# Kernel tuning notes

Hardware: AMD Instinct MI355X
Metric: run time of the kernel (lower is better)

The kernel has to match this reference:

```python
import jax, jax.numpy as jnp
import numpy as np

# Llama-7B FFN up-proj quantized with HQQ 4-bit, group_size=64, axis=0
OUT, IN, GS = 11008, 4096, 64
G = OUT * IN // GS  # 704512 groups


def setup_inputs() -> dict:
    key = jax.random.key(0)
    k1, k2, k3, k4, k5 = jax.random.split(key, 5)
    # packed 4-bit weights: two nibbles per byte, shape [GS//2, G]
    W_q = jax.random.randint(k1, (GS // 2, G), 0, 256, dtype=jnp.int32)
    # per-group scale (meta['scale'] = 1/scale from quantize) and zero
    scale = jax.random.uniform(k2, (1, G), jnp.float32, minval=1e-3, maxval=1e-2)
    zero = jax.random.uniform(k3, (1, G), jnp.float32, minval=0.0, maxval=15.0)
    # decode-style activations: 8 sequences, 1 token each
    x = jax.random.normal(k4, (8, 1, IN), dtype=jnp.float32)
    bias = jax.random.normal(k5, (OUT,), dtype=jnp.float32) * 0.01
    return {"W_q": W_q, "scale": scale, "zero": zero, "x": x, "bias": bias}


def reference(W_q, scale, zero, x, bias):
    # BitPack.unpack_4bit_u8: high nibble rows stacked on low nibble rows
    hi = (W_q >> 4) & 0xF
    lo = W_q & 0xF
    W_q_p = jnp.concatenate([hi, lo], axis=0).astype(x.dtype)  # [GS, G]
    # Quantizer.dequantize: (W_q_p - zero) * scale, reshape to weight shape
    W_r = ((W_q_p - zero) * scale).reshape(OUT, IN)  # [out, in]
    # torch.nn.functional.linear(x, W_r, bias)
    return jnp.einsum('bsi,oi->bso', x, W_r) + bias
```

## Files before the change

### kernel.cpp

```cpp
#include <hip/hip_runtime.h>


#define OUT_ 11008
#define IN_ 4096
#define G_ 704512
#define OC_ 172
#define KS 4
#define KC (IN_ / KS)
#define ITERS (KC / 256)
#define SIB (OC_ * KS)
#define NB (4 * SIB)

__global__ __launch_bounds__(256, 4)
void hqq_gemv(const int* __restrict__ Wq, const float* __restrict__ scale,
              const float* __restrict__ zero, const float* __restrict__ x,
              float* __restrict__ ws) {
    __shared__ float red[128 * 64];

    const int lane = threadIdx.x;
    const int ty   = threadIdx.y;
    const int bid  = blockIdx.x;
    const int bx   = bid / SIB;
    const int rem  = bid % SIB;
    const int oc   = rem >> 2;
    const int ks   = rem & 3;
    const int rq0  = bx * 8 + ty * 2;

    const int kbase = ks * KC;
    const int gb = oc * IN_ + kbase;

    const int* __restrict__ wqA = Wq + (long)rq0 * G_ + gb;
    const int* __restrict__ wqB = wqA + G_;
    int4 qA[ITERS], qB[ITERS];
#pragma unroll
    for (int it = 0; it < ITERS; ++it) {
        qA[it] = *(const int4*)(wqA + it * 256 + lane * 4);
        qB[it] = *(const int4*)(wqB + it * 256 + lane * 4);
    }

    float acc[4][8];
#pragma unroll
    for (int r = 0; r < 4; ++r)
#pragma unroll
        for (int b = 0; b < 8; ++b) acc[r][b] = 0.f;

#pragma unroll
    for (int it = 0; it < ITERS; ++it) {
        const int i = it * 256 + lane * 4;
        const float4 s4 = *(const float4*)(scale + gb + i);
        const float4 z4 = *(const float4*)(zero + gb + i);
        const float ss[4] = {s4.x, s4.y, s4.z, s4.w};
        const float zs[4] = {-z4.x * s4.x, -z4.y * s4.y, -z4.z * s4.z, -z4.w * s4.w};
        const int qsA[4] = {qA[it].x, qA[it].y, qA[it].z, qA[it].w};
        const int qsB[4] = {qB[it].x, qB[it].y, qB[it].z, qB[it].w};

        float w[4][4];
#pragma unroll
        for (int j = 0; j < 4; ++j) {
            w[0][j] = fmaf((float)((qsA[j] >> 4) & 0xF), ss[j], zs[j]);
            w[1][j] = fmaf((float)( qsA[j]       & 0xF), ss[j], zs[j]);
            w[2][j] = fmaf((float)((qsB[j] >> 4) & 0xF), ss[j], zs[j]);
            w[3][j] = fmaf((float)( qsB[j]       & 0xF), ss[j], zs[j]);
        }
#pragma unroll
        for (int b = 0; b < 8; ++b) {
            const float4 xb = *(const float4*)(x + b * IN_ + kbase + i);
#pragma unroll
            for (int r = 0; r < 4; ++r) {
                float a = acc[r][b];
                a = fmaf(xb.x, w[r][0], a);
                a = fmaf(xb.y, w[r][1], a);
                a = fmaf(xb.z, w[r][2], a);
                a = fmaf(xb.w, w[r][3], a);
                acc[r][b] = a;
            }
        }
    }

    const int obase = ty * 32;
#pragma unroll
    for (int r = 0; r < 4; ++r)
#pragma unroll
        for (int b = 0; b < 8; ++b) {
            const int o = obase + r * 8 + b;
            red[o * 64 + (lane ^ ((o & 7) << 3))] = acc[r][b];
        }
    __syncthreads();

    const int t = ty * 64 + lane;
    if (t < 128) {
        const int o = t;
        const int c = (o & 7) << 3;
        float s = 0.f;
#pragma unroll
        for (int j = 0; j < 16; ++j) {
            const float4 v = *(const float4*)(red + o * 64 + ((j * 4) ^ c));
            s += (v.x + v.y) + (v.z + v.w);
        }
        const int w_  = o >> 5;
        const int r   = (o >> 3) & 3;
        const int b   = o & 7;
        const int rq  = bx * 8 + w_ * 2 + (r >> 1);
        const int row = rq + ((r & 1) ? 32 : 0);
        ws[((long)ks * 8 + b) * OUT_ + row * OC_ + oc] = s;
    }
}

__global__ void hqq_reduce(const float* __restrict__ ws,
                           const float* __restrict__ bias,
                           float* __restrict__ out) {
    const int t = blockIdx.x * 256 + threadIdx.x;
    if (t >= 8 * OUT_) return;
    const int o = t % OUT_;
    float v = bias[o];
#pragma unroll
    for (int k = 0; k < KS; ++k) v += ws[k * 8 * OUT_ + t];
    out[t] = v;
}

extern "C" void kernel_launch(void* const* d_in, const int* in_sizes, int n_in,
                              void* d_out, int out_size, void* d_ws, size_t ws_size,
                              hipStream_t stream) {
    const int*   Wq    = (const int*)d_in[0];
    const float* scale = (const float*)d_in[1];
    const float* zero  = (const float*)d_in[2];
    const float* x     = (const float*)d_in[3];
    const float* bias  = (const float*)d_in[4];
    float* out = (float*)d_out;
    float* ws  = (float*)d_ws;

    dim3 grid(NB);
    dim3 block(64, 4);
    hqq_gemv<<<grid, block, 0, stream>>>(Wq, scale, zero, x, ws);
    hqq_reduce<<<(8 * OUT_ + 255) / 256, 256, 0, stream>>>(ws, bias, out);
}
```

Baseline: 152.2 us.

## Stage x, scale, zero into LDS via async global_load_lds and coalesce partial writes

Loads the activation slice, scale and zero vectors into shared memory with the direct global-to-LDS load builtin before the main loop, so the per-wave loads that were repeated across the four waves become one shared copy. The LDS buffer is reused for the cross-lane reduction with a modified XOR swizzle. Partial-sum writes become contiguous per block, and the reduce kernel takes over the scattered index mapping. This adds a block-wide barrier and a larger LDS footprint (40KB), which may reduce occupancy below the launch-bounds target.

```diff
diff --git a/kernel.cpp b/kernel.cpp
--- a/kernel.cpp
+++ b/kernel.cpp
@@ -11,14 +11,24 @@
 #define SIB (OC_ * KS)
 #define NB (4 * SIB)
 
+typedef const __attribute__((address_space(1))) void* gptr1_t;
+typedef __attribute__((address_space(3))) void* sptr3_t;
+
+__device__ __forceinline__ void gload_lds16(const float* g, float* l) {
+    __builtin_amdgcn_global_load_lds((gptr1_t)g, (sptr3_t)l, 16, 0, 0);
+}
+
 __global__ __launch_bounds__(256, 4)
 void hqq_gemv(const int* __restrict__ Wq, const float* __restrict__ scale,
               const float* __restrict__ zero, const float* __restrict__ x,
               float* __restrict__ ws) {
-    __shared__ float red[128 * 64];
+    __shared__ float x_lds[8 * KC];
+    __shared__ float s_lds[KC];
+    __shared__ float z_lds[KC];
 
     const int lane = threadIdx.x;
     const int ty   = threadIdx.y;
+    const int tid  = ty * 64 + lane;
     const int bid  = blockIdx.x;
     const int bx   = bid / SIB;
     const int rem  = bid % SIB;
@@ -29,6 +39,14 @@
     const int kbase = ks * KC;
     const int gb = oc * IN_ + kbase;
 
+    const int wf = ty * 256;
+    gload_lds16(scale + gb + wf + lane * 4, s_lds + wf);
+    gload_lds16(zero  + gb + wf + lane * 4, z_lds + wf);
+#pragma unroll
+    for (int r = 0; r < 8; ++r) {
+        gload_lds16(x + r * IN_ + kbase + wf + lane * 4, x_lds + r * 1024 + wf);
+    }
+
     const int* __restrict__ wqA = Wq + (long)rq0 * G_ + gb;
     const int* __restrict__ wqB = wqA + G_;
     int4 qA[ITERS], qB[ITERS];
@@ -37,6 +55,8 @@
         qA[it] = *(const int4*)(wqA + it * 256 + lane * 4);
         qB[it] = *(const int4*)(wqB + it * 256 + lane * 4);
     }
+
+    __syncthreads();
 
     float acc[4][8];
 #pragma unroll
@@ -47,8 +67,8 @@
 #pragma unroll
     for (int it = 0; it < ITERS; ++it) {
         const int i = it * 256 + lane * 4;
-        const float4 s4 = *(const float4*)(scale + gb + i);
-        const float4 z4 = *(const float4*)(zero + gb + i);
+        const float4 s4 = *(const float4*)(s_lds + i);
+        const float4 z4 = *(const float4*)(z_lds + i);
         const float ss[4] = {s4.x, s4.y, s4.z, s4.w};
         const float zs[4] = {-z4.x * s4.x, -z4.y * s4.y, -z4.z * s4.z, -z4.w * s4.w};
         const int qsA[4] = {qA[it].x, qA[it].y, qA[it].z, qA[it].w};
@@ -64,7 +84,7 @@
         }
 #pragma unroll
         for (int b = 0; b < 8; ++b) {
-            const float4 xb = *(const float4*)(x + b * IN_ + kbase + i);
+            const float4 xb = *(const float4*)(x_lds + b * KC + i);
 #pragma unroll
             for (int r = 0; r < 4; ++r) {
                 float a = acc[r][b];
@@ -77,32 +97,28 @@
         }
     }
 
+    float* red = x_lds;
+    __syncthreads();
     const int obase = ty * 32;
 #pragma unroll
     for (int r = 0; r < 4; ++r)
 #pragma unroll
         for (int b = 0; b < 8; ++b) {
             const int o = obase + r * 8 + b;
-            red[o * 64 + (lane ^ ((o & 7) << 3))] = acc[r][b];
+            red[o * 64 + (lane ^ ((o & 7) << 2))] = acc[r][b];
         }
     __syncthreads();
 
-    const int t = ty * 64 + lane;
-    if (t < 128) {
-        const int o = t;
-        const int c = (o & 7) << 3;
+    if (tid < 128) {
+        const int o = tid;
+        const int c = (o & 7) << 2;
         float s = 0.f;
 #pragma unroll
         for (int j = 0; j < 16; ++j) {
             const float4 v = *(const float4*)(red + o * 64 + ((j * 4) ^ c));
             s += (v.x + v.y) + (v.z + v.w);
         }
-        const int w_  = o >> 5;
-        const int r   = (o >> 3) & 3;
-        const int b   = o & 7;
-        const int rq  = bx * 8 + w_ * 2 + (r >> 1);
-        const int row = rq + ((r & 1) ? 32 : 0);
-        ws[((long)ks * 8 + b) * OUT_ + row * OC_ + oc] = s;
+        ws[(long)((bx * OC_ + oc) * KS + ks) * 128 + o] = s;
     }
 }
 
@@ -112,9 +128,18 @@
     const int t = blockIdx.x * 256 + threadIdx.x;
     if (t >= 8 * OUT_) return;
     const int o = t % OUT_;
+    const int b = t / OUT_;
+    const int row = o / OC_;
+    const int oc  = o % OC_;
+    const int rq  = row & 31;
+    const int hi  = row >> 5;
+    const int bx  = rq >> 3;
+    const int w_  = (rq >> 1) & 3;
+    const int r   = ((rq & 1) << 1) | hi;
+    const int base = ((bx * OC_ + oc) * KS) * 128 + w_ * 32 + r * 8 + b;
     float v = bias[o];
 #pragma unroll
-    for (int k = 0; k < KS; ++k) v += ws[k * 8 * OUT_ + t];
+    for (int k = 0; k < KS; ++k) v += ws[base + k * 128];
     out[t] = v;
 }
 
```

After: 144.9 us (median of 3 runs). 1.05x faster.

## Use single-wave blocks with XCD-aware chunk mapping and double-buffered loads

Applied to the files above, without the earlier changes.

Shrinks each block to one 64-thread wave and remaps block ids so that all 16 row-pair waves sharing a (oc, ks) chunk land on the same XCD. The aim is for them to share scale, zero and x data in that XCD's L2. The up-front load of every weight vector is replaced by a two-stage register double buffer that also prefetches scale and zero. The workspace layout changes to be chunk-major, so the reduce kernel now recovers output indices itself. This trades more, smaller blocks and less memory-level parallelism per wave for better L2 locality and lower register pressure.

```diff
diff --git a/kernel.cpp b/kernel.cpp
--- a/kernel.cpp
+++ b/kernel.cpp
@@ -8,35 +8,40 @@
 #define KS 4
 #define KC (IN_ / KS)
 #define ITERS (KC / 256)
-#define SIB (OC_ * KS)
-#define NB (4 * SIB)
+#define NCHUNK (OC_ * KS)
+#define NB (NCHUNK * 16)
 
-__global__ __launch_bounds__(256, 4)
+__global__ __launch_bounds__(64, 4)
 void hqq_gemv(const int* __restrict__ Wq, const float* __restrict__ scale,
               const float* __restrict__ zero, const float* __restrict__ x,
               float* __restrict__ ws) {
-    __shared__ float red[128 * 64];
+    __shared__ float red[32 * 64];
 
     const int lane = threadIdx.x;
-    const int ty   = threadIdx.y;
     const int bid  = blockIdx.x;
-    const int bx   = bid / SIB;
-    const int rem  = bid % SIB;
-    const int oc   = rem >> 2;
-    const int ks   = rem & 3;
-    const int rq0  = bx * 8 + ty * 2;
+    const int xcd  = bid & 7;
+    const int i_   = bid >> 3;
+    const int c    = xcd * (NCHUNK / 8) + (i_ >> 4);
+    const int sib  = i_ & 15;
+    const int oc   = c >> 2;
+    const int ks   = c & 3;
+    const int rq0  = sib * 2;
 
     const int kbase = ks * KC;
-    const int gb = oc * IN_ + kbase;
+    const int gb    = oc * IN_ + kbase;
 
-    const int* __restrict__ wqA = Wq + (long)rq0 * G_ + gb;
-    const int* __restrict__ wqB = wqA + G_;
-    int4 qA[ITERS], qB[ITERS];
-#pragma unroll
-    for (int it = 0; it < ITERS; ++it) {
-        qA[it] = *(const int4*)(wqA + it * 256 + lane * 4);
-        qB[it] = *(const int4*)(wqB + it * 256 + lane * 4);
-    }
+    const int*   __restrict__ wqA = Wq + (long)rq0 * G_ + gb + lane * 4;
+    const int*   __restrict__ wqB = wqA + G_;
+    const float* __restrict__ sp  = scale + gb + lane * 4;
+    const float* __restrict__ zp  = zero  + gb + lane * 4;
+    const float* __restrict__ xp  = x + kbase + lane * 4;
+
+    int4   qa[2], qb[2];
+    float4 sv[2], zv[2];
+    qa[0] = *(const int4*)(wqA);
+    qb[0] = *(const int4*)(wqB);
+    sv[0] = *(const float4*)(sp);
+    zv[0] = *(const float4*)(zp);
 
     float acc[4][8];
 #pragma unroll
@@ -46,13 +51,19 @@
 
 #pragma unroll
     for (int it = 0; it < ITERS; ++it) {
-        const int i = it * 256 + lane * 4;
-        const float4 s4 = *(const float4*)(scale + gb + i);
-        const float4 z4 = *(const float4*)(zero + gb + i);
+        const int cur = it & 1, nxt = cur ^ 1;
+        if (it + 1 < ITERS) {
+            qa[nxt] = *(const int4*)(wqA + (it + 1) * 256);
+            qb[nxt] = *(const int4*)(wqB + (it + 1) * 256);
+            sv[nxt] = *(const float4*)(sp + (it + 1) * 256);
+            zv[nxt] = *(const float4*)(zp + (it + 1) * 256);
+        }
+        const float4 s4 = sv[cur];
+        const float4 z4 = zv[cur];
         const float ss[4] = {s4.x, s4.y, s4.z, s4.w};
         const float zs[4] = {-z4.x * s4.x, -z4.y * s4.y, -z4.z * s4.z, -z4.w * s4.w};
-        const int qsA[4] = {qA[it].x, qA[it].y, qA[it].z, qA[it].w};
-        const int qsB[4] = {qB[it].x, qB[it].y, qB[it].z, qB[it].w};
+        const int qsA[4] = {qa[cur].x, qa[cur].y, qa[cur].z, qa[cur].w};
+        const int qsB[4] = {qb[cur].x, qb[cur].y, qb[cur].z, qb[cur].w};
 
         float w[4][4];
 #pragma unroll
@@ -64,7 +75,7 @@
         }
 #pragma unroll
         for (int b = 0; b < 8; ++b) {
-            const float4 xb = *(const float4*)(x + b * IN_ + kbase + i);
+            const float4 xb = *(const float4*)(xp + b * IN_ + it * 256);
 #pragma unroll
             for (int r = 0; r < 4; ++r) {
                 float a = acc[r][b];
@@ -77,45 +88,46 @@
         }
     }
 
-    const int obase = ty * 32;
 #pragma unroll
     for (int r = 0; r < 4; ++r)
 #pragma unroll
         for (int b = 0; b < 8; ++b) {
-            const int o = obase + r * 8 + b;
-            red[o * 64 + (lane ^ ((o & 7) << 3))] = acc[r][b];
+            const int o = r * 8 + b;
+            red[o * 64 + (lane ^ ((o & 7) << 2))] = acc[r][b];
         }
     __syncthreads();
 
-    const int t = ty * 64 + lane;
-    if (t < 128) {
-        const int o = t;
-        const int c = (o & 7) << 3;
-        float s = 0.f;
+    const int o    = lane >> 1;
+    const int half = lane & 1;
+    const int cc   = (o & 7) << 2;
+    float v = 0.f;
 #pragma unroll
-        for (int j = 0; j < 16; ++j) {
-            const float4 v = *(const float4*)(red + o * 64 + ((j * 4) ^ c));
-            s += (v.x + v.y) + (v.z + v.w);
-        }
-        const int w_  = o >> 5;
-        const int r   = (o >> 3) & 3;
-        const int b   = o & 7;
-        const int rq  = bx * 8 + w_ * 2 + (r >> 1);
-        const int row = rq + ((r & 1) ? 32 : 0);
-        ws[((long)ks * 8 + b) * OUT_ + row * OC_ + oc] = s;
+    for (int j = 0; j < 8; ++j) {
+        const float4 t = *(const float4*)(red + o * 64 + half * 32 + ((j * 4) ^ cc));
+        v += (t.x + t.y) + (t.z + t.w);
     }
+    v += __shfl_down(v, 1, 64);
+    if (half == 0)
+        ws[(c << 9) + (sib << 5) + o] = v;
 }
 
 __global__ void hqq_reduce(const float* __restrict__ ws,
                            const float* __restrict__ bias,
                            float* __restrict__ out) {
     const int t = blockIdx.x * 256 + threadIdx.x;
-    if (t >= 8 * OUT_) return;
-    const int o = t % OUT_;
-    float v = bias[o];
+    if (t >= OC_ * 512) return;
+    const int oc = t >> 9;
+    const int u  = t & 511;
+    const int base = (oc << 2 << 9) + u;
+    float v = 0.f;
 #pragma unroll
-    for (int k = 0; k < KS; ++k) v += ws[k * 8 * OUT_ + t];
-    out[t] = v;
+    for (int k = 0; k < KS; ++k) v += ws[base + (k << 9)];
+    const int sib = u >> 5;
+    const int r   = (u >> 3) & 3;
+    const int b   = u & 7;
+    const int row = sib * 2 + (r >> 1) + (r & 1) * 32;
+    const int oo  = row * OC_ + oc;
+    out[b * OUT_ + oo] = v + bias[oo];
 }
 
 extern "C" void kernel_launch(void* const* d_in, const int* in_sizes, int n_in,
@@ -130,7 +142,7 @@
     float* ws  = (float*)d_ws;
 
     dim3 grid(NB);
-    dim3 block(64, 4);
+    dim3 block(64);
     hqq_gemv<<<grid, block, 0, stream>>>(Wq, scale, zero, x, ws);
-    hqq_reduce<<<(8 * OUT_ + 255) / 256, 256, 0, stream>>>(ws, bias, out);
+    hqq_reduce<<<(OC_ * 512 + 255) / 256, 256, 0, stream>>>(ws, bias, out);
 }
```

Result: slower. 159.2 us (+4.6%).
